# Optimization experiments

Hardware: AMD Instinct MI355X
Metric: run time of the kernel (lower is better)

## Reference

```python
import jax, jax.numpy as jnp
import numpy as np

N, FEAT, H, D, E, C = 3072, 512, 8, 8, 100000, 2
ALPHA = 0.2  # LeakyReLU slope
NEG_INF = -9e15


def setup_inputs() -> dict:
    key = jax.random.key(0)
    ks = jax.random.split(key, 12)
    x = jax.random.normal(ks[0], (N, FEAT), dtype=jnp.float32)
    adj = (jax.random.uniform(ks[1], (N, N)) < 0.002).astype(jnp.float32)
    adj = jnp.maximum(adj, jnp.eye(N, dtype=jnp.float32))
    L = jax.random.randint(ks[2], (E,), 0, N)
    R = jax.random.randint(ks[3], (E,), 0, N)
    label = jax.random.randint(ks[4], (E,), 0, C)
    s = 1.0 / np.sqrt(FEAT)
    W = jax.random.uniform(ks[5], (H, FEAT, D), minval=-s, maxval=s, dtype=jnp.float32)
    sa = 1.0 / np.sqrt(2 * D)
    a1 = jax.random.uniform(ks[6], (H, D), minval=-sa, maxval=sa, dtype=jnp.float32)
    a2 = jax.random.uniform(ks[7], (H, D), minval=-sa, maxval=sa, dtype=jnp.float32)
    s1 = 1.0 / np.sqrt(H * D * 2)
    W1 = jax.random.uniform(ks[8], (H * D * 2, 64), minval=-s1, maxval=s1, dtype=jnp.float32)
    b1 = jnp.zeros((64,), dtype=jnp.float32)
    s2 = 1.0 / np.sqrt(64)
    W2 = jax.random.uniform(ks[9], (64, C), minval=-s2, maxval=s2, dtype=jnp.float32)
    b2 = jnp.zeros((C,), dtype=jnp.float32)
    return {"x": x, "adj": adj, "L": L, "R": R, "label": label,
            "W": W, "a1": a1, "a2": a2, "W1": W1, "b1": b1, "W2": W2, "b2": b2}


def _encoder(x, adj, W, a1, a2):
    # Wh: [H, N, D]
    Wh = jnp.einsum('nf,hfd->hnd', x, W)
    # broadcast attention logits: e[h,i,j] = leaky_relu(Wh_i.a1 + Wh_j.a2)
    s1 = jnp.einsum('hnd,hd->hn', Wh, a1)[:, :, None]   # [H,N,1]
    s2 = jnp.einsum('hnd,hd->hn', Wh, a2)[:, None, :]   # [H,1,N]
    e = jax.nn.leaky_relu(s1 + s2, negative_slope=ALPHA)  # [H,N,N]
    e = jnp.where(adj[None] > 0, e, NEG_INF)
    att = jax.nn.softmax(e, axis=-1)                      # [H,N,N]
    h = jnp.einsum('hnm,hmd->hnd', att, Wh)               # [H,N,D]
    h = jax.nn.elu(h)                                     # concat=True -> ELU
    # concat heads: [N, H*D]
    return jnp.transpose(h, (1, 0, 2)).reshape(x.shape[0], -1)


def reference(x, adj, L, R, label, W, a1, a2, W1, b1, W2, b2):
    emb = _encoder(x, adj, W, a1, a2)            # [N, 64]
    lr = jnp.concatenate([emb[L], emb[R]], axis=1)  # [E, 128]
    hcls = jax.nn.relu(lr @ W1 + b1)
    logits = hcls @ W2 + b2                       # [E, C]
    logp = jax.nn.log_softmax(logits, axis=-1)
    nll = -jnp.take_along_axis(logp, label[:, None], axis=1)[:, 0]
    return jnp.mean(nll)
```

## Files before the change

### kernel.cpp

```cpp
#include <hip/hip_runtime.h>
#include <math.h>

#define NN 3072
#define FEAT 512
#define HD 64
#define NE 100000
#define ALPHA 0.2f
#define CAP 96
#define CAPP 97
#define K5_BLOCKS 2048

__global__ __launch_bounds__(64) void k_pre(const float* __restrict__ adj, const float* __restrict__ W,
                                            int* __restrict__ nbr, int* __restrict__ cnt,
                                            float* __restrict__ Wt2) {
    int i = blockIdx.x;
    int lane = threadIdx.x;
    if (i < (FEAT * HD) / 64) {
        int idx = i * 64 + lane;
        int f = idx >> 6, hd = idx & 63;
        Wt2[((f >> 2) * HD + hd) * 4 + (f & 3)] = W[(hd >> 3) * FEAT * 8 + f * 8 + (hd & 7)];
    }
    const float4* row = (const float4*)&adj[(size_t)i * NN];
    float4 v[12];
    #pragma unroll
    for (int c = 0; c < 12; ++c) v[c] = row[c * 64 + lane];
    unsigned long long lmask = (1ull << lane) - 1ull;
    int base = 0;
    #pragma unroll
    for (int c = 0; c < 12; ++c) {
        #pragma unroll
        for (int k = 0; k < 4; ++k) {
            float vk = k == 0 ? v[c].x : k == 1 ? v[c].y : k == 2 ? v[c].z : v[c].w;
            bool nz = vk > 0.f;
            unsigned long long m = __ballot(nz);
            if (nz) {
                int pos = base + __popcll(m & lmask);
                if (pos < CAP) nbr[i * CAP + pos] = c * 256 + lane * 4 + k;
            }
            base += __popcll(m);
        }
    }
    if (lane == 0) cnt[i] = base < CAP ? base : CAP;
}

__global__ __launch_bounds__(512) void k_wh(const float* __restrict__ x, const float4* __restrict__ Wt2v,
                                            const float* __restrict__ a1, const float* __restrict__ a2,
                                            float* __restrict__ Wh, float* __restrict__ s1t,
                                            float* __restrict__ s2t) {
    __shared__ float4 xs4[4][FEAT / 4];
    __shared__ float part[8][4][HD];
    int n0 = blockIdx.x * 4;
    int tid = threadIdx.x;
    {
        int r = tid >> 7, fq = tid & 127;
        xs4[r][fq] = ((const float4*)x)[(n0 + r) * (FEAT / 4) + fq];
    }
    __syncthreads();
    int w = tid >> 6, l = tid & 63;
    float acc0 = 0.f, acc1 = 0.f, acc2 = 0.f, acc3 = 0.f;
    #pragma unroll 4
    for (int i4 = 0; i4 < 16; ++i4) {
        int fq = w * 16 + i4;
        float4 wt = Wt2v[fq * HD + l];
        float4 x0 = xs4[0][fq], x1 = xs4[1][fq], x2 = xs4[2][fq], x3 = xs4[3][fq];
        acc0 = fmaf(x0.x, wt.x, fmaf(x0.y, wt.y, fmaf(x0.z, wt.z, fmaf(x0.w, wt.w, acc0))));
        acc1 = fmaf(x1.x, wt.x, fmaf(x1.y, wt.y, fmaf(x1.z, wt.z, fmaf(x1.w, wt.w, acc1))));
        acc2 = fmaf(x2.x, wt.x, fmaf(x2.y, wt.y, fmaf(x2.z, wt.z, fmaf(x2.w, wt.w, acc2))));
        acc3 = fmaf(x3.x, wt.x, fmaf(x3.y, wt.y, fmaf(x3.z, wt.z, fmaf(x3.w, wt.w, acc3))));
    }
    part[w][0][l] = acc0;
    part[w][1][l] = acc1;
    part[w][2][l] = acc2;
    part[w][3][l] = acc3;
    __syncthreads();
    if (w < 4) {
        int n = n0 + w;
        float v = 0.f;
        #pragma unroll
        for (int w2 = 0; w2 < 8; ++w2) v += part[w2][w][l];
        Wh[n * HD + l] = v;
        float t1 = v * a1[l];
        float t2 = v * a2[l];
        for (int m = 1; m < 8; m <<= 1) {
            t1 += __shfl_xor(t1, m, 64);
            t2 += __shfl_xor(t2, m, 64);
        }
        if ((l & 7) == 0) {
            int h = l >> 3;
            s1t[n * 8 + h] = t1;
            s2t[n * 8 + h] = t2;
        }
    }
}

__global__ __launch_bounds__(256) void k_attn_pq(const float* __restrict__ Wh, const float* __restrict__ s1t,
                                                 const float* __restrict__ s2t, const int* __restrict__ nbr,
                                                 const int* __restrict__ cnt, const float* __restrict__ W1,
                                                 const float* __restrict__ b1, float* __restrict__ P,
                                                 float* __restrict__ Q) {
    __shared__ int   jbuf[4][CAP];
    __shared__ float ebuf[4][8][CAPP];
    __shared__ float es[4][HD];
    int wid = threadIdx.x >> 6;
    int lane = threadIdx.x & 63;
    int i = blockIdx.x * 4 + wid;
    int h = lane >> 3, d = lane & 7;
    int ni = cnt[i];
    for (int k = lane; k < CAP; k += 64)
        if (k < ni) jbuf[wid][k] = nbr[i * CAP + k];
    __syncthreads();
    float s1i = s1t[i * 8 + h];
    float mloc = -INFINITY;
    for (int k = d; k < ni; k += 8) {
        int j = jbuf[wid][k];
        float ev = s1i + s2t[j * 8 + h];
        ev = ev > 0.f ? ev : ALPHA * ev;
        ebuf[wid][h][k] = ev;
        mloc = fmaxf(mloc, ev);
    }
    mloc = fmaxf(mloc, __shfl_xor(mloc, 1, 8));
    mloc = fmaxf(mloc, __shfl_xor(mloc, 2, 8));
    mloc = fmaxf(mloc, __shfl_xor(mloc, 4, 8));
    __syncthreads();
    float denom = 0.f, acc = 0.f;
    for (int k = 0; k < ni; ++k) {
        float p = __expf(ebuf[wid][h][k] - mloc);
        denom += p;
        acc = fmaf(p, Wh[jbuf[wid][k] * HD + lane], acc);
    }
    float o = acc / denom;
    o = o > 0.f ? o : expm1f(o);
    es[wid][lane] = o;
    __syncthreads();
    float p = b1[lane], q = 0.f;
    #pragma unroll 8
    for (int k = 0; k < HD; ++k) {
        float e = es[wid][k];
        p = fmaf(e, W1[k * HD + lane], p);
        q = fmaf(e, W1[(HD + k) * HD + lane], q);
    }
    P[i * HD + lane] = p;
    Q[i * HD + lane] = q;
}

__global__ __launch_bounds__(256) void k_cls(const float* __restrict__ P, const float* __restrict__ Q,
                                             const int* __restrict__ L, const int* __restrict__ R,
                                             const int* __restrict__ label, const float* __restrict__ W2,
                                             const float* __restrict__ b2, float* __restrict__ partials) {
    int tid = threadIdx.x;
    int sl = tid & 15;
    int grp = (blockIdx.x * 256 + tid) >> 4;
    int ngrp = gridDim.x * 16;
    float2 wa = *(const float2*)&W2[(sl * 4 + 0) * 2];
    float2 wb = *(const float2*)&W2[(sl * 4 + 1) * 2];
    float2 wc = *(const float2*)&W2[(sl * 4 + 2) * 2];
    float2 wd = *(const float2*)&W2[(sl * 4 + 3) * 2];
    float b20 = b2[0], b21 = b2[1];
    float sum = 0.f;
    for (int e = grp; e < NE; e += ngrp) {
        int ln = L[e], rn = R[e];
        float4 p = *(const float4*)&P[ln * HD + sl * 4];
        float4 q = *(const float4*)&Q[rn * HD + sl * 4];
        float v0 = fmaxf(p.x + q.x, 0.f);
        float v1 = fmaxf(p.y + q.y, 0.f);
        float v2 = fmaxf(p.z + q.z, 0.f);
        float v3 = fmaxf(p.w + q.w, 0.f);
        float t0 = v0 * wa.x + v1 * wb.x + v2 * wc.x + v3 * wd.x;
        float t1 = v0 * wa.y + v1 * wb.y + v2 * wc.y + v3 * wd.y;
        #pragma unroll
        for (int m = 1; m < 16; m <<= 1) {
            t0 += __shfl_xor(t0, m, 64);
            t1 += __shfl_xor(t1, m, 64);
        }
        if (sl == 0) {
            float l0 = t0 + b20, l1 = t1 + b21;
            float mx = fmaxf(l0, l1);
            float lse = mx + __logf(__expf(l0 - mx) + __expf(l1 - mx));
            float sel = label[e] ? l1 : l0;
            sum += lse - sel;
        }
    }
    __shared__ float red[256];
    red[tid] = sum;
    __syncthreads();
    for (int s = 128; s > 0; s >>= 1) {
        if (tid < s) red[tid] += red[tid + s];
        __syncthreads();
    }
    if (tid == 0) partials[blockIdx.x] = red[0];
}

__global__ __launch_bounds__(1024) void k_reduce(const float* __restrict__ partials, float* __restrict__ out) {
    __shared__ float sh[1024];
    int t = threadIdx.x;
    sh[t] = partials[t] + partials[t + 1024];
    __syncthreads();
    for (int s = 512; s > 0; s >>= 1) {
        if (t < s) sh[t] += sh[t + s];
        __syncthreads();
    }
    if (t == 0) out[0] = sh[0] / (float)NE;
}

extern "C" void kernel_launch(void* const* d_in, const int* in_sizes, int n_in,
                              void* d_out, int out_size, void* d_ws, size_t ws_size,
                              hipStream_t stream) {
    const float* x     = (const float*)d_in[0];
    const float* adj   = (const float*)d_in[1];
    const int*   L     = (const int*)d_in[2];
    const int*   R     = (const int*)d_in[3];
    const int*   label = (const int*)d_in[4];
    const float* W     = (const float*)d_in[5];
    const float* a1    = (const float*)d_in[6];
    const float* a2    = (const float*)d_in[7];
    const float* W1    = (const float*)d_in[8];
    const float* b1    = (const float*)d_in[9];
    const float* W2    = (const float*)d_in[10];
    const float* b2    = (const float*)d_in[11];

    char* ws = (char*)d_ws;
    float* Wt2      = (float*)(ws + 0);
    float* Wh       = (float*)(ws + 131072);
    float* s1t      = (float*)(ws + 917504);
    float* s2t      = (float*)(ws + 1015808);
    int*   cnt      = (int*)  (ws + 1114112);
    int*   nbr      = (int*)  (ws + 1126400);
    float* P        = (float*)(ws + 2306048);
    float* Q        = (float*)(ws + 3092480);
    float* partials = (float*)(ws + 0);

    k_pre<<<NN, 64, 0, stream>>>(adj, W, nbr, cnt, Wt2);
    k_wh<<<NN / 4, 512, 0, stream>>>(x, (const float4*)Wt2, a1, a2, Wh, s1t, s2t);
    k_attn_pq<<<NN / 4, 256, 0, stream>>>(Wh, s1t, s2t, nbr, cnt, W1, b1, P, Q);
    k_cls<<<K5_BLOCKS, 256, 0, stream>>>(P, Q, L, R, label, W2, b2, partials);
    k_reduce<<<1, 1024, 0, stream>>>(partials, (float*)d_out);
}
```

Baseline: 38.39 us.

## Fuse adjacency scan with Wh projection and fold final reduction into classifier

Merges the adjacency-compaction kernel and the Wh projection kernel into one launch. Odd blocks scan adjacency rows and even blocks compute Wh, reading W directly and dropping the separate W transpose. The final reduction kernel is removed: the last classifier block, found with an atomic counter, sums all partials. This cuts two launches and the transpose work, at the cost of strided uncoalesced W reads, atomics, and a counter reset that depends on the kernels running in stream order.

Measured after the change: 97.09 us. 153% more time.

```diff
diff --git a/kernel.cpp b/kernel.cpp
--- a/kernel.cpp
+++ b/kernel.cpp
@@ -10,83 +10,76 @@
 #define CAPP 97
 #define K5_BLOCKS 2048
 
-__global__ __launch_bounds__(64) void k_pre(const float* __restrict__ adj, const float* __restrict__ W,
-                                            int* __restrict__ nbr, int* __restrict__ cnt,
-                                            float* __restrict__ Wt2) {
-    int i = blockIdx.x;
-    int lane = threadIdx.x;
-    if (i < (FEAT * HD) / 64) {
-        int idx = i * 64 + lane;
-        int f = idx >> 6, hd = idx & 63;
-        Wt2[((f >> 2) * HD + hd) * 4 + (f & 3)] = W[(hd >> 3) * FEAT * 8 + f * 8 + (hd & 7)];
-    }
-    const float4* row = (const float4*)&adj[(size_t)i * NN];
-    float4 v[12];
-    #pragma unroll
-    for (int c = 0; c < 12; ++c) v[c] = row[c * 64 + lane];
-    unsigned long long lmask = (1ull << lane) - 1ull;
-    int base = 0;
-    #pragma unroll
-    for (int c = 0; c < 12; ++c) {
+__global__ __launch_bounds__(256) void k_stage1(const float* __restrict__ adj, const float* __restrict__ x,
+                                                const float* __restrict__ W, const float* __restrict__ a1,
+                                                const float* __restrict__ a2, int* __restrict__ nbr,
+                                                int* __restrict__ cnt, float* __restrict__ Wh,
+                                                float* __restrict__ s1t, float* __restrict__ s2t,
+                                                unsigned* __restrict__ counter) {
+    __shared__ float xs[4][FEAT];
+    __shared__ float part[4][4][HD];
+    int b = blockIdx.x;
+    int tid = threadIdx.x;
+    if (b == 0 && tid == 0) counter[0] = 0;
+    int wid = tid >> 6, lane = tid & 63;
+
+    if (b & 1) {
+        int i = (b >> 1) * 4 + wid;
+        const float4* row = (const float4*)&adj[(size_t)i * NN];
+        float4 v[12];
         #pragma unroll
-        for (int k = 0; k < 4; ++k) {
-            float vk = k == 0 ? v[c].x : k == 1 ? v[c].y : k == 2 ? v[c].z : v[c].w;
-            bool nz = vk > 0.f;
-            unsigned long long m = __ballot(nz);
-            if (nz) {
-                int pos = base + __popcll(m & lmask);
-                if (pos < CAP) nbr[i * CAP + pos] = c * 256 + lane * 4 + k;
+        for (int c = 0; c < 12; ++c) v[c] = row[c * 64 + lane];
+        unsigned long long lmask = (1ull << lane) - 1ull;
+        int base = 0;
+        #pragma unroll
+        for (int c = 0; c < 12; ++c) {
+            #pragma unroll
+            for (int k = 0; k < 4; ++k) {
+                float vk = k == 0 ? v[c].x : k == 1 ? v[c].y : k == 2 ? v[c].z : v[c].w;
+                bool nz = vk > 0.f;
+                unsigned long long m = __ballot(nz);
+                if (nz) {
+                    int pos = base + __popcll(m & lmask);
+                    if (pos < CAP) nbr[i * CAP + pos] = c * 256 + lane * 4 + k;
+                }
+                base += __popcll(m);
             }
-            base += __popcll(m);
-        }
-    }
-    if (lane == 0) cnt[i] = base < CAP ? base : CAP;
-}
-
-__global__ __launch_bounds__(512) void k_wh(const float* __restrict__ x, const float4* __restrict__ Wt2v,
-                                            const float* __restrict__ a1, const float* __restrict__ a2,
-                                            float* __restrict__ Wh, float* __restrict__ s1t,
-                                            float* __restrict__ s2t) {
-    __shared__ float4 xs4[4][FEAT / 4];
-    __shared__ float part[8][4][HD];
-    int n0 = blockIdx.x * 4;
-    int tid = threadIdx.x;
-    {
-        int r = tid >> 7, fq = tid & 127;
-        xs4[r][fq] = ((const float4*)x)[(n0 + r) * (FEAT / 4) + fq];
-    }
-    __syncthreads();
-    int w = tid >> 6, l = tid & 63;
-    float acc0 = 0.f, acc1 = 0.f, acc2 = 0.f, acc3 = 0.f;
-    #pragma unroll 4
-    for (int i4 = 0; i4 < 16; ++i4) {
-        int fq = w * 16 + i4;
-        float4 wt = Wt2v[fq * HD + l];
-        float4 x0 = xs4[0][fq], x1 = xs4[1][fq], x2 = xs4[2][fq], x3 = xs4[3][fq];
-        acc0 = fmaf(x0.x, wt.x, fmaf(x0.y, wt.y, fmaf(x0.z, wt.z, fmaf(x0.w, wt.w, acc0))));
-        acc1 = fmaf(x1.x, wt.x, fmaf(x1.y, wt.y, fmaf(x1.z, wt.z, fmaf(x1.w, wt.w, acc1))));
-        acc2 = fmaf(x2.x, wt.x, fmaf(x2.y, wt.y, fmaf(x2.z, wt.z, fmaf(x2.w, wt.w, acc2))));
-        acc3 = fmaf(x3.x, wt.x, fmaf(x3.y, wt.y, fmaf(x3.z, wt.z, fmaf(x3.w, wt.w, acc3))));
-    }
-    part[w][0][l] = acc0;
-    part[w][1][l] = acc1;
-    part[w][2][l] = acc2;
-    part[w][3][l] = acc3;
-    __syncthreads();
-    if (w < 4) {
-        int n = n0 + w;
-        float v = 0.f;
-        #pragma unroll
-        for (int w2 = 0; w2 < 8; ++w2) v += part[w2][w][l];
-        Wh[n * HD + l] = v;
-        float t1 = v * a1[l];
-        float t2 = v * a2[l];
+        }
+        if (lane == 0) cnt[i] = base < CAP ? base : CAP;
+    } else {
+        int n0 = (b >> 1) * 4;
+        for (int idx = tid; idx < 512; idx += 256) {
+            int r = idx >> 7, fq = idx & 127;
+            *(float4*)&xs[r][fq * 4] = ((const float4*)x)[(size_t)(n0 + r) * (FEAT / 4) + fq];
+        }
+        __syncthreads();
+        const float* wp = W + (lane >> 3) * (FEAT * 8) + (lane & 7);
+        int f0 = wid * (FEAT / 4);
+        float acc0 = 0.f, acc1 = 0.f, acc2 = 0.f, acc3 = 0.f;
+        #pragma unroll 8
+        for (int f = f0; f < f0 + FEAT / 4; ++f) {
+            float wt = wp[f * 8];
+            acc0 = fmaf(xs[0][f], wt, acc0);
+            acc1 = fmaf(xs[1][f], wt, acc1);
+            acc2 = fmaf(xs[2][f], wt, acc2);
+            acc3 = fmaf(xs[3][f], wt, acc3);
+        }
+        part[wid][0][lane] = acc0;
+        part[wid][1][lane] = acc1;
+        part[wid][2][lane] = acc2;
+        part[wid][3][lane] = acc3;
+        __syncthreads();
+        int n = n0 + wid;
+        float v = part[0][wid][lane] + part[1][wid][lane] + part[2][wid][lane] + part[3][wid][lane];
+        Wh[n * HD + lane] = v;
+        float t1 = v * a1[lane];
+        float t2 = v * a2[lane];
         for (int m = 1; m < 8; m <<= 1) {
             t1 += __shfl_xor(t1, m, 64);
             t2 += __shfl_xor(t2, m, 64);
         }
-        if ((l & 7) == 0) {
-            int h = l >> 3;
+        if ((lane & 7) == 0) {
+            int h = lane >> 3;
             s1t[n * 8 + h] = t1;
             s2t[n * 8 + h] = t2;
         }
@@ -146,7 +139,8 @@
 __global__ __launch_bounds__(256) void k_cls(const float* __restrict__ P, const float* __restrict__ Q,
                                              const int* __restrict__ L, const int* __restrict__ R,
                                              const int* __restrict__ label, const float* __restrict__ W2,
-                                             const float* __restrict__ b2, float* __restrict__ partials) {
+                                             const float* __restrict__ b2, float* __restrict__ partials,
+                                             unsigned* __restrict__ counter, float* __restrict__ out) {
     int tid = threadIdx.x;
     int sl = tid & 15;
     int grp = (blockIdx.x * 256 + tid) >> 4;
@@ -181,25 +175,32 @@
         }
     }
     __shared__ float red[256];
+    __shared__ int lastflag;
     red[tid] = sum;
     __syncthreads();
     for (int s = 128; s > 0; s >>= 1) {
         if (tid < s) red[tid] += red[tid + s];
         __syncthreads();
     }
-    if (tid == 0) partials[blockIdx.x] = red[0];
-}
-
-__global__ __launch_bounds__(1024) void k_reduce(const float* __restrict__ partials, float* __restrict__ out) {
-    __shared__ float sh[1024];
-    int t = threadIdx.x;
-    sh[t] = partials[t] + partials[t + 1024];
-    __syncthreads();
-    for (int s = 512; s > 0; s >>= 1) {
-        if (t < s) sh[t] += sh[t + s];
-        __syncthreads();
-    }
-    if (t == 0) out[0] = sh[0] / (float)NE;
+    if (tid == 0) {
+        __hip_atomic_store(&partials[blockIdx.x], red[0], __ATOMIC_RELEASE, __HIP_MEMORY_SCOPE_AGENT);
+        unsigned old = __hip_atomic_fetch_add(counter, 1u, __ATOMIC_ACQ_REL, __HIP_MEMORY_SCOPE_AGENT);
+        lastflag = (old == (unsigned)(gridDim.x - 1));
+    }
+    __syncthreads();
+    if (lastflag) {
+        float s = 0.f;
+        for (int k = tid; k < K5_BLOCKS; k += 256)
+            s += __hip_atomic_load(&partials[k], __ATOMIC_ACQUIRE, __HIP_MEMORY_SCOPE_AGENT);
+        __syncthreads();
+        red[tid] = s;
+        __syncthreads();
+        for (int s2 = 128; s2 > 0; s2 >>= 1) {
+            if (tid < s2) red[tid] += red[tid + s2];
+            __syncthreads();
+        }
+        if (tid == 0) out[0] = red[0] / (float)NE;
+    }
 }
 
 extern "C" void kernel_launch(void* const* d_in, const int* in_sizes, int n_in,
@@ -219,19 +220,17 @@
     const float* b2    = (const float*)d_in[11];
 
     char* ws = (char*)d_ws;
-    float* Wt2      = (float*)(ws + 0);
-    float* Wh       = (float*)(ws + 131072);
-    float* s1t      = (float*)(ws + 917504);
-    float* s2t      = (float*)(ws + 1015808);
-    int*   cnt      = (int*)  (ws + 1114112);
-    int*   nbr      = (int*)  (ws + 1126400);
-    float* P        = (float*)(ws + 2306048);
-    float* Q        = (float*)(ws + 3092480);
-    float* partials = (float*)(ws + 0);
-
-    k_pre<<<NN, 64, 0, stream>>>(adj, W, nbr, cnt, Wt2);
-    k_wh<<<NN / 4, 512, 0, stream>>>(x, (const float4*)Wt2, a1, a2, Wh, s1t, s2t);
+    float*    Wh       = (float*)   (ws + 0);
+    float*    s1t      = (float*)   (ws + 786432);
+    float*    s2t      = (float*)   (ws + 884736);
+    int*      cnt      = (int*)     (ws + 983040);
+    int*      nbr      = (int*)     (ws + 995328);
+    float*    P        = (float*)   (ws + 2174976);
+    float*    Q        = (float*)   (ws + 2961408);
+    float*    partials = (float*)   (ws + 3747840);
+    unsigned* counter  = (unsigned*)(ws + 3756032);
+
+    k_stage1<<<2 * (NN / 4), 256, 0, stream>>>(adj, x, W, a1, a2, nbr, cnt, Wh, s1t, s2t, counter);
     k_attn_pq<<<NN / 4, 256, 0, stream>>>(Wh, s1t, s2t, nbr, cnt, W1, b1, P, Q);
-    k_cls<<<K5_BLOCKS, 256, 0, stream>>>(P, Q, L, R, label, W2, b2, partials);
-    k_reduce<<<1, 1024, 0, stream>>>(partials, (float*)d_out);
-}
+    k_cls<<<K5_BLOCKS, 256, 0, stream>>>(P, Q, L, R, label, W2, b2, partials, counter, (float*)d_out);
+}
```
